# Optimization experiments

Measured on AMD Instinct MI355X. Metric: run time of the kernel, lower is better.

## Reference

```python
import jax, jax.numpy as jnp
import numpy as np

W = 16          # hidden width
N_HIDDEN = 8    # number of 16->16 hidden layers (num_layers - 1)
N_PTS = 2097152


def setup_inputs() -> dict:
    key = jax.random.key(0)
    ks = jax.random.split(key, 7)
    x = jax.random.uniform(ks[0], (N_PTS, 3), dtype=jnp.float32) * 2.0 - 1.0
    # nn.init.normal_ -> std-normal weights; biases left at (small) values
    W0 = jax.random.normal(ks[1], (W, 3), dtype=jnp.float32)
    b0 = jnp.zeros((W,), dtype=jnp.float32)
    Wh = jax.random.normal(ks[2], (N_HIDDEN, W, W), dtype=jnp.float32)
    bh = jnp.zeros((N_HIDDEN, W), dtype=jnp.float32)
    Wo = jax.random.normal(ks[3], (1, W), dtype=jnp.float32)
    bo = jnp.zeros((1,), dtype=jnp.float32)
    return {"x": x, "W0": W0, "b0": b0, "Wh": Wh, "bh": bh, "Wo": Wo, "bo": bo}


def reference(x, W0, b0, Wh, bh, Wo, bo):
    # Linear(3,16) + tanh
    h = jnp.tanh(x @ W0.T + b0)                     # [N, 16]
    def step(h, wb):
        w, b = wb
        return jnp.tanh(h @ w.T + b), None
    h, _ = jax.lax.scan(step, h, (Wh, bh))
    # Linear(16,1) + sigmoid
    return jax.nn.sigmoid(h @ Wo.T + bo)            # [N, 1]
```

## Files before the change

kernel.cpp:

```cpp
#include <hip/hip_runtime.h>

typedef __attribute__((ext_vector_type(4))) _Float16 half4;
typedef __attribute__((ext_vector_type(4))) float floatx4;
typedef __attribute__((ext_vector_type(2))) unsigned uint2v;

#define NH 8
#define CHUNKS 8

struct Split2 { unsigned hi, lo; };

__device__ __forceinline__ Split2 split2(float t0, float t1) {
    unsigned hp = __builtin_bit_cast(unsigned, __builtin_amdgcn_cvt_pkrtz(t0, t1));
    float h0 = (float)__builtin_bit_cast(_Float16, (unsigned short)(hp & 0xffffu));
    float h1 = (float)__builtin_bit_cast(_Float16, (unsigned short)(hp >> 16));
    float l0 = (t0 - h0) * 2048.0f;
    float l1 = (t1 - h1) * 2048.0f;
    Split2 r;
    r.hi = hp;
    r.lo = __builtin_bit_cast(unsigned, __builtin_amdgcn_cvt_pkrtz(l0, l1));
    return r;
}

__device__ __forceinline__ floatx4 quad_r(float s0, float s1, float s2, float s3) {
    s0 = fminf(s0, 25.0f); s1 = fminf(s1, 25.0f);
    s2 = fminf(s2, 25.0f); s3 = fminf(s3, 25.0f);
    float p0 = __builtin_amdgcn_exp2f(s0) + 1.0f;
    float p1 = __builtin_amdgcn_exp2f(s1) + 1.0f;
    float p2 = __builtin_amdgcn_exp2f(s2) + 1.0f;
    float p3 = __builtin_amdgcn_exp2f(s3) + 1.0f;
    float A = p0 * p1, B = p2 * p3;
    float P = A * B;
    float rp = __builtin_amdgcn_rcpf(P);
    rp = rp * fmaf(-P, rp, 2.0f);
    float rA = rp * B, rB = rp * A;
    floatx4 r;
    r[0] = rA * p1; r[1] = rA * p0; r[2] = rB * p3; r[3] = rB * p2;
    return r;
}

__device__ __forceinline__ void split_w(float w, float& hi, float& lo) {
    _Float16 h = (_Float16)w;
    hi = (float)h;
    lo = (w - hi) * 2048.0f;
}

__global__ __launch_bounds__(256, 4) void cppn_kernel(
    const float* __restrict__ x,
    const float* __restrict__ W0,
    const float* __restrict__ b0,
    const float* __restrict__ Wh,
    const float* __restrict__ bh,
    const float* __restrict__ Wo,
    const float* __restrict__ bo,
    float* __restrict__ out)
{
    const int tid  = threadIdx.x;
    const int lane = tid & 63;
    const int col  = lane & 15;
    const int kg   = lane >> 4;
    const int wib  = tid >> 6;

    const float TSCL = 2.8853900817779268f;
    const float NSCL = -2.0f * TSCL;
    const float OSCL = -1.4426950408889634f;
    const float UNSC = 4.8828125e-4f;

    half4   wAhi[NH], wAlo[NH];
    floatx4 bC[NH];
    #pragma unroll
    for (int l = 0; l < NH; ++l) {
        const float* wrow = Wh + l*256 + col*16 + kg*4;
        float w0 = wrow[0], w1 = wrow[1], w2 = wrow[2], w3 = wrow[3];
        float rs = (w0 + w1) + (w2 + w3);
        rs += __shfl_xor(rs, 16);
        rs += __shfl_xor(rs, 32);
        float h0,h1,h2,h3, lo0,lo1,lo2,lo3;
        split_w(w0*NSCL, h0, lo0);
        split_w(w1*NSCL, h1, lo1);
        split_w(w2*NSCL, h2, lo2);
        split_w(w3*NSCL, h3, lo3);
        uint2v ha, la;
        ha.x = __builtin_bit_cast(unsigned, __builtin_amdgcn_cvt_pkrtz(h0, h1));
        ha.y = __builtin_bit_cast(unsigned, __builtin_amdgcn_cvt_pkrtz(h2, h3));
        la.x = __builtin_bit_cast(unsigned, __builtin_amdgcn_cvt_pkrtz(lo0, lo1));
        la.y = __builtin_bit_cast(unsigned, __builtin_amdgcn_cvt_pkrtz(lo2, lo3));
        wAhi[l] = __builtin_bit_cast(half4, ha);
        wAlo[l] = __builtin_bit_cast(half4, la);
        floatx4 c;
        #pragma unroll
        for (int r = 0; r < 4; ++r) {
            float rs_r = __shfl(rs, kg*4 + r);
            c[r] = TSCL * (bh[l*16 + kg*4 + r] + rs_r);
        }
        bC[l] = c;
    }

    float w0r[4][3]; float b0r[4];
    #pragma unroll
    for (int r = 0; r < 4; ++r) {
        const float* wp = W0 + (kg*4 + r)*3;
        w0r[r][0] = wp[0]*TSCL; w0r[r][1] = wp[1]*TSCL; w0r[r][2] = wp[2]*TSCL;
        b0r[r] = b0[kg*4 + r]*TSCL;
    }

    float woP[4];
    float wsum;
    {
        const float* wp = Wo + kg*4;
        float a = wp[0], b = wp[1], c2 = wp[2], d = wp[3];
        wsum = (a + b) + (c2 + d);
        wsum += __shfl_xor(wsum, 16);
        wsum += __shfl_xor(wsum, 32);
        woP[0] = a*(-2.0f*OSCL); woP[1] = b*(-2.0f*OSCL);
        woP[2] = c2*(-2.0f*OSCL); woP[3] = d*(-2.0f*OSCL);
    }
    const float boP = OSCL * (bo[0] + wsum);

    const floatx4 zeroC = {0.0f, 0.0f, 0.0f, 0.0f};
    const long base0 = ((long)blockIdx.x * 4 + wib) * (64L * CHUNKS);

    #pragma unroll 1
    for (int c = 0; c < CHUNKS; ++c) {
        const long base = base0 + (long)c * 64;

        half4 hBhi[4], hBlo[4];
        #pragma unroll
        for (int t = 0; t < 4; ++t) {
            const long p = base + t*16 + col;
            const float x0 = x[p*3+0], x1 = x[p*3+1], x2 = x[p*3+2];
            float a0 = fmaf(w0r[0][0],x0, fmaf(w0r[0][1],x1, fmaf(w0r[0][2],x2, b0r[0])));
            float a1 = fmaf(w0r[1][0],x0, fmaf(w0r[1][1],x1, fmaf(w0r[1][2],x2, b0r[1])));
            float a2 = fmaf(w0r[2][0],x0, fmaf(w0r[2][1],x1, fmaf(w0r[2][2],x2, b0r[2])));
            float a3 = fmaf(w0r[3][0],x0, fmaf(w0r[3][1],x1, fmaf(w0r[3][2],x2, b0r[3])));
            floatx4 rq = quad_r(a0, a1, a2, a3);
            Split2 p01 = split2(rq[0], rq[1]);
            Split2 p23 = split2(rq[2], rq[3]);
            uint2v hb, lb;
            hb.x = p01.hi; hb.y = p23.hi;
            lb.x = p01.lo; lb.y = p23.lo;
            hBhi[t] = __builtin_bit_cast(half4, hb);
            hBlo[t] = __builtin_bit_cast(half4, lb);
        }

        #pragma unroll
        for (int l = 0; l < NH-1; ++l) {
            const half4 whi = wAhi[l];
            const half4 wlo = wAlo[l];
            const floatx4 bc = bC[l];
            #pragma unroll
            for (int tp = 0; tp < 2; ++tp) {
                const int u0 = tp*2, u1 = tp*2+1;
                floatx4 d0 = __builtin_amdgcn_mfma_f32_16x16x16f16(whi, hBhi[u0], bc, 0,0,0);
                floatx4 d1 = __builtin_amdgcn_mfma_f32_16x16x16f16(whi, hBhi[u1], bc, 0,0,0);
                floatx4 e0 = __builtin_amdgcn_mfma_f32_16x16x16f16(whi, hBlo[u0], zeroC, 0,0,0);
                floatx4 e1 = __builtin_amdgcn_mfma_f32_16x16x16f16(whi, hBlo[u1], zeroC, 0,0,0);
                e0 = __builtin_amdgcn_mfma_f32_16x16x16f16(wlo, hBhi[u0], e0, 0,0,0);
                e1 = __builtin_amdgcn_mfma_f32_16x16x16f16(wlo, hBhi[u1], e1, 0,0,0);

                floatx4 q0 = quad_r(fmaf(e0[0], UNSC, d0[0]),
                                    fmaf(e0[1], UNSC, d0[1]),
                                    fmaf(e0[2], UNSC, d0[2]),
                                    fmaf(e0[3], UNSC, d0[3]));
                floatx4 q1 = quad_r(fmaf(e1[0], UNSC, d1[0]),
                                    fmaf(e1[1], UNSC, d1[1]),
                                    fmaf(e1[2], UNSC, d1[2]),
                                    fmaf(e1[3], UNSC, d1[3]));
                Split2 a01 = split2(q0[0], q0[1]);
                Split2 a23 = split2(q0[2], q0[3]);
                Split2 b01 = split2(q1[0], q1[1]);
                Split2 b23 = split2(q1[2], q1[3]);
                uint2v hb0, lb0, hb1, lb1;
                hb0.x = a01.hi; hb0.y = a23.hi;
                lb0.x = a01.lo; lb0.y = a23.lo;
                hb1.x = b01.hi; hb1.y = b23.hi;
                lb1.x = b01.lo; lb1.y = b23.lo;
                hBhi[u0] = __builtin_bit_cast(half4, hb0);
                hBlo[u0] = __builtin_bit_cast(half4, lb0);
                hBhi[u1] = __builtin_bit_cast(half4, hb1);
                hBlo[u1] = __builtin_bit_cast(half4, lb1);
            }
        }

        float tot[4];
        #pragma unroll
        for (int t = 0; t < 4; ++t) {
            floatx4 d = __builtin_amdgcn_mfma_f32_16x16x16f16(wAhi[NH-1], hBhi[t], bC[NH-1], 0,0,0);
            floatx4 e = __builtin_amdgcn_mfma_f32_16x16x16f16(wAhi[NH-1], hBlo[t], zeroC, 0,0,0);
            e = __builtin_amdgcn_mfma_f32_16x16x16f16(wAlo[NH-1], hBhi[t], e, 0,0,0);
            floatx4 r8 = quad_r(fmaf(e[0], UNSC, d[0]),
                                fmaf(e[1], UNSC, d[1]),
                                fmaf(e[2], UNSC, d[2]),
                                fmaf(e[3], UNSC, d[3]));
            float acc = fmaf(woP[0], r8[0],
                        fmaf(woP[1], r8[1],
                        fmaf(woP[2], r8[2], woP[3] * r8[3])));
            acc += __shfl_xor(acc, 16);
            acc += __shfl_xor(acc, 32);
            tot[t] = acc;
        }

        float s = (kg == 0) ? tot[0] : (kg == 1) ? tot[1] : (kg == 2) ? tot[2] : tot[3];
        s += boP;
        float E = __builtin_amdgcn_exp2f(s);
        out[base + lane] = __builtin_amdgcn_rcpf(1.0f + E);
    }
}

extern "C" void kernel_launch(void* const* d_in, const int* in_sizes, int n_in,
                              void* d_out, int out_size, void* d_ws, size_t ws_size,
                              hipStream_t stream) {
    const float* x  = (const float*)d_in[0];
    const float* W0 = (const float*)d_in[1];
    const float* b0 = (const float*)d_in[2];
    const float* Wh = (const float*)d_in[3];
    const float* bh = (const float*)d_in[4];
    const float* Wo = (const float*)d_in[5];
    const float* bo = (const float*)d_in[6];
    float* out = (float*)d_out;

    int n = out_size;
    int block = 256;
    long ptsPerBlock = 4L * 64 * CHUNKS;
    int grid = (int)((n + ptsPerBlock - 1) / ptsPerBlock);
    cppn_kernel<<<grid, block, 0, stream>>>(x, W0, b0, Wh, bh, Wo, bo, out);
}
```

Before: 107.3 us.

## Merge hi/lo correction MFMAs into one 16x16x32 MFMA, drop Newton step

Packs each layer's hi and lo weight halves into one 8-wide fp16 operand. The two 16x16x16 correction MFMAs (whi*hlo + wlo*hhi) become a single 16x16x32 MFMA, with the B operand built from the concatenated lo and hi activations. This cuts the matrix instruction count per layer and removes the dependent accumulate chain. It also drops the Newton refinement after the reciprocal in the tanh helper and switches index arithmetic from 64-bit to 32-bit, trading some accuracy and extra register packing moves for fewer instructions.

```diff
diff --git a/kernel.cpp b/kernel.cpp
--- a/kernel.cpp
+++ b/kernel.cpp
@@ -1,8 +1,10 @@
 #include <hip/hip_runtime.h>
 
 typedef __attribute__((ext_vector_type(4))) _Float16 half4;
+typedef __attribute__((ext_vector_type(8))) _Float16 half8;
 typedef __attribute__((ext_vector_type(4))) float floatx4;
 typedef __attribute__((ext_vector_type(2))) unsigned uint2v;
+typedef __attribute__((ext_vector_type(4))) unsigned uint4v;
 
 #define NH 8
 #define CHUNKS 8
@@ -31,7 +33,6 @@
     float A = p0 * p1, B = p2 * p3;
     float P = A * B;
     float rp = __builtin_amdgcn_rcpf(P);
-    rp = rp * fmaf(-P, rp, 2.0f);
     float rA = rp * B, rB = rp * A;
     floatx4 r;
     r[0] = rA * p1; r[1] = rA * p0; r[2] = rB * p3; r[3] = rB * p2;
@@ -65,7 +66,7 @@
     const float OSCL = -1.4426950408889634f;
     const float UNSC = 4.8828125e-4f;
 
-    half4   wAhi[NH], wAlo[NH];
+    half8   wA8[NH];
     floatx4 bC[NH];
     #pragma unroll
     for (int l = 0; l < NH; ++l) {
@@ -79,13 +80,12 @@
         split_w(w1*NSCL, h1, lo1);
         split_w(w2*NSCL, h2, lo2);
         split_w(w3*NSCL, h3, lo3);
-        uint2v ha, la;
-        ha.x = __builtin_bit_cast(unsigned, __builtin_amdgcn_cvt_pkrtz(h0, h1));
-        ha.y = __builtin_bit_cast(unsigned, __builtin_amdgcn_cvt_pkrtz(h2, h3));
-        la.x = __builtin_bit_cast(unsigned, __builtin_amdgcn_cvt_pkrtz(lo0, lo1));
-        la.y = __builtin_bit_cast(unsigned, __builtin_amdgcn_cvt_pkrtz(lo2, lo3));
-        wAhi[l] = __builtin_bit_cast(half4, ha);
-        wAlo[l] = __builtin_bit_cast(half4, la);
+        uint4v wa;
+        wa.x = __builtin_bit_cast(unsigned, __builtin_amdgcn_cvt_pkrtz(h0, h1));
+        wa.y = __builtin_bit_cast(unsigned, __builtin_amdgcn_cvt_pkrtz(h2, h3));
+        wa.z = __builtin_bit_cast(unsigned, __builtin_amdgcn_cvt_pkrtz(lo0, lo1));
+        wa.w = __builtin_bit_cast(unsigned, __builtin_amdgcn_cvt_pkrtz(lo2, lo3));
+        wA8[l] = __builtin_bit_cast(half8, wa);
         floatx4 c;
         #pragma unroll
         for (int r = 0; r < 4; ++r) {
@@ -117,16 +117,16 @@
     const float boP = OSCL * (bo[0] + wsum);
 
     const floatx4 zeroC = {0.0f, 0.0f, 0.0f, 0.0f};
-    const long base0 = ((long)blockIdx.x * 4 + wib) * (64L * CHUNKS);
+    const int base0 = (blockIdx.x * 4 + wib) * (64 * CHUNKS);
 
     #pragma unroll 1
     for (int c = 0; c < CHUNKS; ++c) {
-        const long base = base0 + (long)c * 64;
+        const int base = base0 + c * 64;
 
         half4 hBhi[4], hBlo[4];
         #pragma unroll
         for (int t = 0; t < 4; ++t) {
-            const long p = base + t*16 + col;
+            const int p = base + t*16 + col;
             const float x0 = x[p*3+0], x1 = x[p*3+1], x2 = x[p*3+2];
             float a0 = fmaf(w0r[0][0],x0, fmaf(w0r[0][1],x1, fmaf(w0r[0][2],x2, b0r[0])));
             float a1 = fmaf(w0r[1][0],x0, fmaf(w0r[1][1],x1, fmaf(w0r[1][2],x2, b0r[1])));
@@ -144,18 +144,25 @@
 
         #pragma unroll
         for (int l = 0; l < NH-1; ++l) {
-            const half4 whi = wAhi[l];
-            const half4 wlo = wAlo[l];
+            const half8 wa8 = wA8[l];
+            const uint4v wau = __builtin_bit_cast(uint4v, wa8);
+            uint2v whu; whu.x = wau.x; whu.y = wau.y;
+            const half4 whi = __builtin_bit_cast(half4, whu);
             const floatx4 bc = bC[l];
             #pragma unroll
             for (int tp = 0; tp < 2; ++tp) {
                 const int u0 = tp*2, u1 = tp*2+1;
+                const uint2v hbu0 = __builtin_bit_cast(uint2v, hBhi[u0]);
+                const uint2v lbu0 = __builtin_bit_cast(uint2v, hBlo[u0]);
+                const uint2v hbu1 = __builtin_bit_cast(uint2v, hBhi[u1]);
+                const uint2v lbu1 = __builtin_bit_cast(uint2v, hBlo[u1]);
+                uint4v b0v, b1v;
+                b0v.x = lbu0.x; b0v.y = lbu0.y; b0v.z = hbu0.x; b0v.w = hbu0.y;
+                b1v.x = lbu1.x; b1v.y = lbu1.y; b1v.z = hbu1.x; b1v.w = hbu1.y;
                 floatx4 d0 = __builtin_amdgcn_mfma_f32_16x16x16f16(whi, hBhi[u0], bc, 0,0,0);
                 floatx4 d1 = __builtin_amdgcn_mfma_f32_16x16x16f16(whi, hBhi[u1], bc, 0,0,0);
-                floatx4 e0 = __builtin_amdgcn_mfma_f32_16x16x16f16(whi, hBlo[u0], zeroC, 0,0,0);
-                floatx4 e1 = __builtin_amdgcn_mfma_f32_16x16x16f16(whi, hBlo[u1], zeroC, 0,0,0);
-                e0 = __builtin_amdgcn_mfma_f32_16x16x16f16(wlo, hBhi[u0], e0, 0,0,0);
-                e1 = __builtin_amdgcn_mfma_f32_16x16x16f16(wlo, hBhi[u1], e1, 0,0,0);
+                floatx4 e0 = __builtin_amdgcn_mfma_f32_16x16x32_f16(wa8, __builtin_bit_cast(half8, b0v), zeroC, 0,0,0);
+                floatx4 e1 = __builtin_amdgcn_mfma_f32_16x16x32_f16(wa8, __builtin_bit_cast(half8, b1v), zeroC, 0,0,0);
 
                 floatx4 q0 = quad_r(fmaf(e0[0], UNSC, d0[0]),
                                     fmaf(e0[1], UNSC, d0[1]),
@@ -182,21 +189,31 @@
         }
 
         float tot[4];
-        #pragma unroll
-        for (int t = 0; t < 4; ++t) {
-            floatx4 d = __builtin_amdgcn_mfma_f32_16x16x16f16(wAhi[NH-1], hBhi[t], bC[NH-1], 0,0,0);
-            floatx4 e = __builtin_amdgcn_mfma_f32_16x16x16f16(wAhi[NH-1], hBlo[t], zeroC, 0,0,0);
-            e = __builtin_amdgcn_mfma_f32_16x16x16f16(wAlo[NH-1], hBhi[t], e, 0,0,0);
-            floatx4 r8 = quad_r(fmaf(e[0], UNSC, d[0]),
-                                fmaf(e[1], UNSC, d[1]),
-                                fmaf(e[2], UNSC, d[2]),
-                                fmaf(e[3], UNSC, d[3]));
-            float acc = fmaf(woP[0], r8[0],
-                        fmaf(woP[1], r8[1],
-                        fmaf(woP[2], r8[2], woP[3] * r8[3])));
-            acc += __shfl_xor(acc, 16);
-            acc += __shfl_xor(acc, 32);
-            tot[t] = acc;
+        {
+            const half8 wa8 = wA8[NH-1];
+            const uint4v wau = __builtin_bit_cast(uint4v, wa8);
+            uint2v whu; whu.x = wau.x; whu.y = wau.y;
+            const half4 whi = __builtin_bit_cast(half4, whu);
+            const floatx4 bc = bC[NH-1];
+            #pragma unroll
+            for (int t = 0; t < 4; ++t) {
+                const uint2v hbu = __builtin_bit_cast(uint2v, hBhi[t]);
+                const uint2v lbu = __builtin_bit_cast(uint2v, hBlo[t]);
+                uint4v bv;
+                bv.x = lbu.x; bv.y = lbu.y; bv.z = hbu.x; bv.w = hbu.y;
+                floatx4 d = __builtin_amdgcn_mfma_f32_16x16x16f16(whi, hBhi[t], bc, 0,0,0);
+                floatx4 e = __builtin_amdgcn_mfma_f32_16x16x32_f16(wa8, __builtin_bit_cast(half8, bv), zeroC, 0,0,0);
+                floatx4 r8 = quad_r(fmaf(e[0], UNSC, d[0]),
+                                    fmaf(e[1], UNSC, d[1]),
+                                    fmaf(e[2], UNSC, d[2]),
+                                    fmaf(e[3], UNSC, d[3]));
+                float acc = fmaf(woP[0], r8[0],
+                            fmaf(woP[1], r8[1],
+                            fmaf(woP[2], r8[2], woP[3] * r8[3])));
+                acc += __shfl_xor(acc, 16);
+                acc += __shfl_xor(acc, 32);
+                tot[t] = acc;
+            }
         }
 
         float s = (kg == 0) ? tot[0] : (kg == 1) ? tot[1] : (kg == 2) ? tot[2] : tot[3];
```

Result: no change. 107.1 us (-0.1%).
